# Performance work log

Measured on AMD Instinct MI355X. Metric: run time of the kernel, lower is better.

Reference implementation:

```python
import jax, jax.numpy as jnp
import numpy as np

B, CIN, H, W = 32, 128, 64, 64
OUT, KH, KW = 256, 3, 3
NSK, SDIM = 4, 128


def setup_inputs() -> dict:
    key = jax.random.key(0)
    kx, kw_, kb, ks = jax.random.split(key, 4)
    x = jax.random.normal(kx, (B, CIN, H, W), dtype=jnp.float32)
    kval = float(np.sqrt(1.0 / (CIN * KH * KW)))  # groups=1
    weight = jax.random.uniform(kw_, (OUT, CIN, KH, KW), jnp.float32, -kval, kval)
    bias_tensor = jax.random.uniform(kb, (OUT,), jnp.float32, -kval, kval)
    # Rademacher / sketch_dim, shape (n, s, O) == torch's type1_signed_matrices
    signed = (2.0 * jax.random.bernoulli(ks, 0.5, (NSK, SDIM, OUT)).astype(jnp.float32) - 1.0) / SDIM
    # prod = einsum('ijkl,mi->mjkl') per sketch -> (n, s, Cin, kh, kw)
    prod = jnp.einsum('oikl,nso->nsikl', weight, signed)
    # .permute(2,3,1,0).flatten(0,2): (s,Cin,kh,kw) -> (kh,kw,Cin,s) -> (kh*kw*Cin, s)
    type1_sketches = prod.transpose(0, 3, 4, 2, 1).reshape(NSK, KH * KW * CIN, SDIM)
    return {
        "x": x,
        "type1_sketches": type1_sketches,
        "type1_signed_matrices": signed,
        "bias_tensor": bias_tensor,
    }


def reference(x, type1_sketches, type1_signed_matrices, bias_tensor):
    b, _, h1, w1 = x.shape
    h2 = h1 - KH + 1
    w2 = w1 - KW + 1
    # torch unfold: (B, Cin*KH*KW, E), features ordered channel-major (C, kh, kw)
    patches = jax.lax.conv_general_dilated_patches(
        x, filter_shape=(KH, KW), window_strides=(1, 1), padding='VALID'
    )  # (B, Cin*KH*KW, H2, W2)
    patches = patches.reshape(b, CIN * KH * KW, h2 * w2)  # (B, F, E)
    # 'bnfe,nfs->bnse' with the n-expansion folded away
    y = jnp.einsum('bfe,nfs->bnse', patches, type1_sketches)
    z = jnp.einsum('bnse,nso->bnoe', y, type1_signed_matrices)
    z = z.reshape(b, NSK, OUT, h2, w2)
    out = jnp.mean(z, axis=1) + bias_tensor[None, :, None, None]
    return out
```

## Files before the change

kernel.cpp:

```cpp
#include <hip/hip_runtime.h>
#include <hip/hip_bf16.h>
#include <stdint.h>


#define BATCH 32
#define CIN   128
#define HH    64
#define WW    64
#define OUTC  256
#define H2    62
#define W2    62
#define A_TILE 16384
#define WS_A_BYTES (36 * A_TILE)
#define BROWB 16384

typedef __bf16 bf16x8 __attribute__((ext_vector_type(8)));
typedef float  f32x4  __attribute__((ext_vector_type(4)));

typedef unsigned int u32_as1 __attribute__((address_space(1)));
typedef unsigned int u32_as3 __attribute__((address_space(3)));

__device__ __forceinline__ void async_copy16(const void* g, void* l) {
  __builtin_amdgcn_global_load_lds((const u32_as1*)g, (u32_as3*)l, 16, 0, 0);
}

#define FPB 4
__global__ __launch_bounds__(256) void weff_kernel(
    const float* __restrict__ sketches,
    const float* __restrict__ sgn,
    char* __restrict__ wsA)
{
  __shared__ alignas(16) float sk[512 * FPB];
  const int f0 = blockIdx.x * FPB;
  const int t  = threadIdx.x;

  for (int k = 0; k < (512 * FPB) / 256; ++k) {
    int idx = t + k * 256;
    int fi  = idx >> 9;
    int ns  = idx & 511;
    int n   = ns >> 7;
    int s   = ns & 127;
    sk[ns * FPB + fi] = sketches[(n * 1152 + f0 + fi) * 128 + s];
  }
  __syncthreads();

  const int o = t;
  float acc0 = 0.f, acc1 = 0.f, acc2 = 0.f, acc3 = 0.f;
#pragma unroll 8
  for (int ns = 0; ns < 512; ++ns) {
    float sg = sgn[ns * 256 + o];
    f32x4 skv = *(const f32x4*)(&sk[ns * FPB]);
    acc0 += sg * skv[0];
    acc1 += sg * skv[1];
    acc2 += sg * skv[2];
    acc3 += sg * skv[3];
  }

  float accs[FPB] = {acc0, acc1, acc2, acc3};
#pragma unroll
  for (int fi = 0; fi < FPB; ++fi) {
    int f    = f0 + fi;
    int c    = f / 9;
    int khkw = f - c * 9;
    int st   = khkw * 4 + (c >> 5);
    int kk   = c & 31;
    uint32_t byteoff = (uint32_t)st * A_TILE + (uint32_t)o * 64
                     + (((uint32_t)kk * 2u) ^ (uint32_t)((o & 3) << 4)
                                            ^ (uint32_t)((o & 4) << 2));
    *(__hip_bfloat16*)(wsA + byteoff) = __float2bfloat16(accs[fi] * 0.25f);
  }
}

__global__ __launch_bounds__(512, 2) void conv_kernel(
    const float* __restrict__ x,
    const char*  __restrict__ wA,
    const float* __restrict__ bias,
    float* __restrict__ out)
{
  __shared__ alignas(16) char lds[3 * A_TILE + 6 * BROWB];
  char* ldsA = lds;
  char* ldsB = lds + 3 * A_TILE;

  const int bid = blockIdx.x;
  const int swz = (bid & 7) * 64 + (bid >> 3);
  const int b   = swz >> 4;
  const int ig  = swz & 15;
  const int i0  = ig * 4;

  const int t    = threadIdx.x;
  const int lane = t & 63;
  const int w    = t >> 6;
  const int wo   = w >> 2;
  const int we   = w & 3;

#define STAGE_A(ST, BUF) do {                                              \
    const char* asrc_ = wA + (size_t)(ST) * A_TILE + w * 2048 + lane * 16; \
    char* adst_ = ldsA + (BUF) * A_TILE + w * 2048;                        \
    async_copy16(asrc_,         adst_);                                    \
    async_copy16(asrc_ + 1024,  adst_ + 1024);                             \
  } while (0)

  STAGE_A(0, 0);
  STAGE_A(1, 1);

  {
    const int j  = t & 63;
    const int cq = t >> 6;
    const uint32_t swb = (uint32_t)((j & 7) << 4);
#pragma unroll
    for (int r = 0; r < 6; ++r) {
      int xrow = i0 + r; if (xrow > 63) xrow = 63;
      const float* xr = x + (((size_t)(b * CIN + cq * 16)) * HH + xrow) * WW + j;
      char* lrow = ldsB + r * BROWB + j * 256;
#pragma unroll
      for (int g = 0; g < 2; ++g) {
        bf16x8 pk;
#pragma unroll
        for (int cc = 0; cc < 8; ++cc)
          pk[cc] = (__bf16)xr[(size_t)(g * 8 + cc) * (HH * WW)];
        uint32_t c0b = (uint32_t)(cq * 32 + g * 16);
        *(bf16x8*)(lrow + (c0b ^ swb)) = pk;
      }
    }
  }

  f32x4 acc[8][4];
  const f32x4 zf = {0.f, 0.f, 0.f, 0.f};
#pragma unroll
  for (int mi = 0; mi < 8; ++mi)
#pragma unroll
    for (int ni = 0; ni < 4; ++ni)
      acc[mi][ni] = zf;

  const int ln15  = lane & 15;
  const int khi16 = (lane >> 4) << 4;
  const char* pA = ldsA + (wo * 128 + ln15) * 64
                 + (((uint32_t)khi16) ^ ((uint32_t)((ln15 & 3) << 4))
                                      ^ ((uint32_t)((ln15 & 4) << 2)));

#define MKB(COL, PAR) (ldsB + we * BROWB + (COL) * 256                     \
    + (((uint32_t)khi16) ^ ((uint32_t)(((COL) & 3) << 4)))                 \
    + (uint32_t)((((PAR) ^ (((COL) >> 2) & 1)) & 1) * 64))
  const char* pB0E = MKB(ln15 + 0, 0); const char* pB0O = MKB(ln15 + 0, 1);
  const char* pB1E = MKB(ln15 + 1, 0); const char* pB1O = MKB(ln15 + 1, 1);
  const char* pB2E = MKB(ln15 + 2, 0); const char* pB2O = MKB(ln15 + 2, 1);
  const int c30 = (48 + ln15 + 0 > 63) ? 63 : 48 + ln15 + 0;
  const int c31 = (48 + ln15 + 1 > 63) ? 63 : 48 + ln15 + 1;
  const int c32 = (48 + ln15 + 2 > 63) ? 63 : 48 + ln15 + 2;
  const char* pC0E = MKB(c30, 0); const char* pC0O = MKB(c30, 1);
  const char* pC1E = MKB(c31, 0); const char* pC1O = MKB(c31, 1);
  const char* pC2E = MKB(c32, 0); const char* pC2O = MKB(c32, 1);
#undef MKB

  asm volatile("s_waitcnt lgkmcnt(0)" ::: "memory");

#define MFMA_ __builtin_amdgcn_mfma_f32_16x16x32_bf16
#define WVM2 asm volatile("s_waitcnt vmcnt(2)" ::: "memory")
#define WVM0 asm volatile("s_waitcnt vmcnt(0)" ::: "memory")

#define STEP(ST, KH, KW, CSH, PAR, BUF, TGT, WVM) do {                     \
    WVM;                                                                   \
    __builtin_amdgcn_s_barrier();                                          \
    if ((ST) < 34) STAGE_A((ST) + 2, TGT);                                 \
    const int bimm_ = (KH) * BROWB + (CSH) * 128;                          \
    const int aimm_ = (BUF) * A_TILE;                                      \
    bf16x8 b0_ = *(const bf16x8*)(pB##KW##PAR + bimm_);                    \
    bf16x8 b1_ = *(const bf16x8*)(pB##KW##PAR + bimm_ + 4096);             \
    bf16x8 b2_ = *(const bf16x8*)(pB##KW##PAR + bimm_ + 8192);             \
    bf16x8 b3_ = *(const bf16x8*)(pC##KW##PAR + bimm_);                    \
    bf16x8 a0_ = *(const bf16x8*)(pA + aimm_);                             \
    bf16x8 a1_ = *(const bf16x8*)(pA + aimm_ + 1024);                      \
    bf16x8 a2_ = *(const bf16x8*)(pA + aimm_ + 2048);                      \
    bf16x8 a3_ = *(const bf16x8*)(pA + aimm_ + 3072);                      \
    bf16x8 a4_ = *(const bf16x8*)(pA + aimm_ + 4096);                      \
    bf16x8 a5_ = *(const bf16x8*)(pA + aimm_ + 5120);                      \
    bf16x8 a6_ = *(const bf16x8*)(pA + aimm_ + 6144);                      \
    bf16x8 a7_ = *(const bf16x8*)(pA + aimm_ + 7168);                      \
    __builtin_amdgcn_s_setprio(1);                                         \
    acc[0][0] = MFMA_(a0_, b0_, acc[0][0], 0, 0, 0);                       \
    acc[0][1] = MFMA_(a0_, b1_, acc[0][1], 0, 0, 0);                       \
    acc[0][2] = MFMA_(a0_, b2_, acc[0][2], 0, 0, 0);                       \
    acc[0][3] = MFMA_(a0_, b3_, acc[0][3], 0, 0, 0);                       \
    acc[1][0] = MFMA_(a1_, b0_, acc[1][0], 0, 0, 0);                       \
    acc[1][1] = MFMA_(a1_, b1_, acc[1][1], 0, 0, 0);                       \
    acc[1][2] = MFMA_(a1_, b2_, acc[1][2], 0, 0, 0);                       \
    acc[1][3] = MFMA_(a1_, b3_, acc[1][3], 0, 0, 0);                       \
    acc[2][0] = MFMA_(a2_, b0_, acc[2][0], 0, 0, 0);                       \
    acc[2][1] = MFMA_(a2_, b1_, acc[2][1], 0, 0, 0);                       \
    acc[2][2] = MFMA_(a2_, b2_, acc[2][2], 0, 0, 0);                       \
    acc[2][3] = MFMA_(a2_, b3_, acc[2][3], 0, 0, 0);                       \
    acc[3][0] = MFMA_(a3_, b0_, acc[3][0], 0, 0, 0);                       \
    acc[3][1] = MFMA_(a3_, b1_, acc[3][1], 0, 0, 0);                       \
    acc[3][2] = MFMA_(a3_, b2_, acc[3][2], 0, 0, 0);                       \
    acc[3][3] = MFMA_(a3_, b3_, acc[3][3], 0, 0, 0);                       \
    acc[4][0] = MFMA_(a4_, b0_, acc[4][0], 0, 0, 0);                       \
    acc[4][1] = MFMA_(a4_, b1_, acc[4][1], 0, 0, 0);                       \
    acc[4][2] = MFMA_(a4_, b2_, acc[4][2], 0, 0, 0);                       \
    acc[4][3] = MFMA_(a4_, b3_, acc[4][3], 0, 0, 0);                       \
    acc[5][0] = MFMA_(a5_, b0_, acc[5][0], 0, 0, 0);                       \
    acc[5][1] = MFMA_(a5_, b1_, acc[5][1], 0, 0, 0);                       \
    acc[5][2] = MFMA_(a5_, b2_, acc[5][2], 0, 0, 0);                       \
    acc[5][3] = MFMA_(a5_, b3_, acc[5][3], 0, 0, 0);                       \
    acc[6][0] = MFMA_(a6_, b0_, acc[6][0], 0, 0, 0);                       \
    acc[6][1] = MFMA_(a6_, b1_, acc[6][1], 0, 0, 0);                       \
    acc[6][2] = MFMA_(a6_, b2_, acc[6][2], 0, 0, 0);                       \
    acc[6][3] = MFMA_(a6_, b3_, acc[6][3], 0, 0, 0);                       \
    acc[7][0] = MFMA_(a7_, b0_, acc[7][0], 0, 0, 0);                       \
    acc[7][1] = MFMA_(a7_, b1_, acc[7][1], 0, 0, 0);                       \
    acc[7][2] = MFMA_(a7_, b2_, acc[7][2], 0, 0, 0);                       \
    acc[7][3] = MFMA_(a7_, b3_, acc[7][3], 0, 0, 0);                       \
    __builtin_amdgcn_s_setprio(0);                                         \
  } while (0)

  STEP(0,  0,0, 0,E, 0, 2, WVM2);  STEP(1,  0,0, 0,O, 1, 0, WVM2);
  STEP(2,  0,0, 1,E, 2, 1, WVM2);  STEP(3,  0,0, 1,O, 0, 2, WVM2);
  STEP(4,  0,1, 0,E, 1, 0, WVM2);  STEP(5,  0,1, 0,O, 2, 1, WVM2);
  STEP(6,  0,1, 1,E, 0, 2, WVM2);  STEP(7,  0,1, 1,O, 1, 0, WVM2);
  STEP(8,  0,2, 0,E, 2, 1, WVM2);  STEP(9,  0,2, 0,O, 0, 2, WVM2);
  STEP(10, 0,2, 1,E, 1, 0, WVM2);  STEP(11, 0,2, 1,O, 2, 1, WVM2);
  STEP(12, 1,0, 0,E, 0, 2, WVM2);  STEP(13, 1,0, 0,O, 1, 0, WVM2);
  STEP(14, 1,0, 1,E, 2, 1, WVM2);  STEP(15, 1,0, 1,O, 0, 2, WVM2);
  STEP(16, 1,1, 0,E, 1, 0, WVM2);  STEP(17, 1,1, 0,O, 2, 1, WVM2);
  STEP(18, 1,1, 1,E, 0, 2, WVM2);  STEP(19, 1,1, 1,O, 1, 0, WVM2);
  STEP(20, 1,2, 0,E, 2, 1, WVM2);  STEP(21, 1,2, 0,O, 0, 2, WVM2);
  STEP(22, 1,2, 1,E, 1, 0, WVM2);  STEP(23, 1,2, 1,O, 2, 1, WVM2);
  STEP(24, 2,0, 0,E, 0, 2, WVM2);  STEP(25, 2,0, 0,O, 1, 0, WVM2);
  STEP(26, 2,0, 1,E, 2, 1, WVM2);  STEP(27, 2,0, 1,O, 0, 2, WVM2);
  STEP(28, 2,1, 0,E, 1, 0, WVM2);  STEP(29, 2,1, 0,O, 2, 1, WVM2);
  STEP(30, 2,1, 1,E, 0, 2, WVM2);  STEP(31, 2,1, 1,O, 1, 0, WVM2);
  STEP(32, 2,2, 0,E, 2, 1, WVM2);  STEP(33, 2,2, 0,O, 0, 2, WVM2);
  STEP(34, 2,2, 1,E, 1, 0, WVM2);  STEP(35, 2,2, 1,O, 2, 1, WVM0);

#undef STEP
#undef WVM0
#undef WVM2
#undef MFMA_
#undef STAGE_A

  const int jn   = ln15;
  const int g4   = lane >> 4;
  const int irow = i0 + we;
  if (irow < H2) {
#pragma unroll
    for (int mi = 0; mi < 8; ++mi) {
#pragma unroll
      for (int ni = 0; ni < 4; ++ni) {
        const int jj = (ni << 4) + jn;
        if (jj < W2) {
#pragma unroll
          for (int rr = 0; rr < 4; ++rr) {
            const int o = (wo << 7) + (mi << 4) + (g4 << 2) + rr;
            out[(((size_t)b * OUTC + o) * H2 + irow) * W2 + jj] =
                acc[mi][ni][rr] + bias[o];
          }
        }
      }
    }
  }
}

extern "C" void kernel_launch(void* const* d_in, const int* in_sizes, int n_in,
                              void* d_out, int out_size, void* d_ws, size_t ws_size,
                              hipStream_t stream) {
  const float* x        = (const float*)d_in[0];
  const float* sketches = (const float*)d_in[1];
  const float* sgn      = (const float*)d_in[2];
  const float* bias     = (const float*)d_in[3];
  float* out            = (float*)d_out;
  char* wsA             = (char*)d_ws;

  if (ws_size < (size_t)WS_A_BYTES) return;

  weff_kernel<<<1152 / FPB, 256, 0, stream>>>(sketches, sgn, wsA);
  conv_kernel<<<BATCH * 16, 512, 0, stream>>>(x, wsA, bias, out);
}
```

Baseline: 110.0 us.

## Deepen A staging to four LDS buffers and software-pipeline fragment loads

The weight tile staging grows from triple to quadruple buffering, so global-to-LDS copies are issued three stages ahead. LDS fragment reads for the next step now go into a second register set while the current step's MFMAs run, which hides LDS latency behind matrix work. The weight-tile layout is changed to a direct per-lane contiguous layout without the XOR swizzle, which simplifies addressing. The cost is more LDS per block, which may limit two blocks per CU, and double the fragment registers, which raises register pressure under the 512x2 launch bounds.

```diff
diff --git a/kernel.cpp b/kernel.cpp
--- a/kernel.cpp
+++ b/kernel.cpp
@@ -59,14 +59,14 @@
   float accs[FPB] = {acc0, acc1, acc2, acc3};
 #pragma unroll
   for (int fi = 0; fi < FPB; ++fi) {
-    int f    = f0 + fi;
-    int c    = f / 9;
-    int khkw = f - c * 9;
-    int st   = khkw * 4 + (c >> 5);
-    int kk   = c & 31;
-    uint32_t byteoff = (uint32_t)st * A_TILE + (uint32_t)o * 64
-                     + (((uint32_t)kk * 2u) ^ (uint32_t)((o & 3) << 4)
-                                            ^ (uint32_t)((o & 4) << 2));
+    int f   = f0 + fi;
+    int c   = f / 9;
+    int tap = f - c * 9;
+    int st  = tap * 4 + (c >> 5);
+    int kk  = c & 31;
+    uint32_t byteoff = (uint32_t)st * A_TILE + (uint32_t)(o >> 4) * 1024
+                     + (uint32_t)(((kk >> 3) * 16 + (o & 15)) * 16)
+                     + (uint32_t)((kk & 7) * 2);
     *(__hip_bfloat16*)(wsA + byteoff) = __float2bfloat16(accs[fi] * 0.25f);
   }
 }
@@ -77,9 +77,9 @@
     const float* __restrict__ bias,
     float* __restrict__ out)
 {
-  __shared__ alignas(16) char lds[3 * A_TILE + 6 * BROWB];
+  __shared__ alignas(16) char lds[4 * A_TILE + 6 * BROWB];
   char* ldsA = lds;
-  char* ldsB = lds + 3 * A_TILE;
+  char* ldsB = lds + 4 * A_TILE;
 
   const int bid = blockIdx.x;
   const int swz = (bid & 7) * 64 + (bid >> 3);
@@ -102,6 +102,7 @@
 
   STAGE_A(0, 0);
   STAGE_A(1, 1);
+  STAGE_A(2, 2);
 
   {
     const int j  = t & 63;
@@ -134,9 +135,7 @@
 
   const int ln15  = lane & 15;
   const int khi16 = (lane >> 4) << 4;
-  const char* pA = ldsA + (wo * 128 + ln15) * 64
-                 + (((uint32_t)khi16) ^ ((uint32_t)((ln15 & 3) << 4))
-                                      ^ ((uint32_t)((ln15 & 4) << 2)));
+  const char* pA = ldsA + wo * 8192 + lane * 16;
 
 #define MKB(COL, PAR) (ldsB + we * BROWB + (COL) * 256                     \
     + (((uint32_t)khi16) ^ ((uint32_t)(((COL) & 3) << 4)))                 \
@@ -152,89 +151,123 @@
   const char* pC2E = MKB(c32, 0); const char* pC2O = MKB(c32, 1);
 #undef MKB
 
-  asm volatile("s_waitcnt lgkmcnt(0)" ::: "memory");
+  bf16x8 A00, A01, A02, A03, A04, A05, A06, A07, B00, B01, B02, B03;
+  bf16x8 A10, A11, A12, A13, A14, A15, A16, A17, B10, B11, B12, B13;
+
+#define PRE(P, BUF, KH, KW, PAR, CSH) do {                                 \
+    const int ab_ = (BUF) * A_TILE;                                        \
+    A##P##0 = *(const bf16x8*)(pA + ab_);                                  \
+    A##P##1 = *(const bf16x8*)(pA + ab_ + 1024);                           \
+    A##P##2 = *(const bf16x8*)(pA + ab_ + 2048);                           \
+    A##P##3 = *(const bf16x8*)(pA + ab_ + 3072);                           \
+    A##P##4 = *(const bf16x8*)(pA + ab_ + 4096);                           \
+    A##P##5 = *(const bf16x8*)(pA + ab_ + 5120);                           \
+    A##P##6 = *(const bf16x8*)(pA + ab_ + 6144);                           \
+    A##P##7 = *(const bf16x8*)(pA + ab_ + 7168);                           \
+    const int bi_ = (KH) * BROWB + (CSH) * 128;                            \
+    B##P##0 = *(const bf16x8*)(pB##KW##PAR + bi_);                         \
+    B##P##1 = *(const bf16x8*)(pB##KW##PAR + bi_ + 4096);                  \
+    B##P##2 = *(const bf16x8*)(pB##KW##PAR + bi_ + 8192);                  \
+    B##P##3 = *(const bf16x8*)(pC##KW##PAR + bi_);                         \
+  } while (0)
 
 #define MFMA_ __builtin_amdgcn_mfma_f32_16x16x32_bf16
+#define MM(P) do {                                                         \
+    __builtin_amdgcn_s_setprio(1);                                         \
+    acc[0][0] = MFMA_(A##P##0, B##P##0, acc[0][0], 0, 0, 0);               \
+    acc[0][1] = MFMA_(A##P##0, B##P##1, acc[0][1], 0, 0, 0);               \
+    acc[0][2] = MFMA_(A##P##0, B##P##2, acc[0][2], 0, 0, 0);               \
+    acc[0][3] = MFMA_(A##P##0, B##P##3, acc[0][3], 0, 0, 0);               \
+    acc[1][0] = MFMA_(A##P##1, B##P##0, acc[1][0], 0, 0, 0);               \
+    acc[1][1] = MFMA_(A##P##1, B##P##1, acc[1][1], 0, 0, 0);               \
+    acc[1][2] = MFMA_(A##P##1, B##P##2, acc[1][2], 0, 0, 0);               \
+    acc[1][3] = MFMA_(A##P##1, B##P##3, acc[1][3], 0, 0, 0);               \
+    acc[2][0] = MFMA_(A##P##2, B##P##0, acc[2][0], 0, 0, 0);               \
+    acc[2][1] = MFMA_(A##P##2, B##P##1, acc[2][1], 0, 0, 0);               \
+    acc[2][2] = MFMA_(A##P##2, B##P##2, acc[2][2], 0, 0, 0);               \
+    acc[2][3] = MFMA_(A##P##2, B##P##3, acc[2][3], 0, 0, 0);               \
+    acc[3][0] = MFMA_(A##P##3, B##P##0, acc[3][0], 0, 0, 0);               \
+    acc[3][1] = MFMA_(A##P##3, B##P##1, acc[3][1], 0, 0, 0);               \
+    acc[3][2] = MFMA_(A##P##3, B##P##2, acc[3][2], 0, 0, 0);               \
+    acc[3][3] = MFMA_(A##P##3, B##P##3, acc[3][3], 0, 0, 0);               \
+    acc[4][0] = MFMA_(A##P##4, B##P##0, acc[4][0], 0, 0, 0);               \
+    acc[4][1] = MFMA_(A##P##4, B##P##1, acc[4][1], 0, 0, 0);               \
+    acc[4][2] = MFMA_(A##P##4, B##P##2, acc[4][2], 0, 0, 0);               \
+    acc[4][3] = MFMA_(A##P##4, B##P##3, acc[4][3], 0, 0, 0);               \
+    acc[5][0] = MFMA_(A##P##5, B##P##0, acc[5][0], 0, 0, 0);               \
+    acc[5][1] = MFMA_(A##P##5, B##P##1, acc[5][1], 0, 0, 0);               \
+    acc[5][2] = MFMA_(A##P##5, B##P##2, acc[5][2], 0, 0, 0);               \
+    acc[5][3] = MFMA_(A##P##5, B##P##3, acc[5][3], 0, 0, 0);               \
+    acc[6][0] = MFMA_(A##P##6, B##P##0, acc[6][0], 0, 0, 0);               \
+    acc[6][1] = MFMA_(A##P##6, B##P##1, acc[6][1], 0, 0, 0);               \
+    acc[6][2] = MFMA_(A##P##6, B##P##2, acc[6][2], 0, 0, 0);               \
+    acc[6][3] = MFMA_(A##P##6, B##P##3, acc[6][3], 0, 0, 0);               \
+    acc[7][0] = MFMA_(A##P##7, B##P##0, acc[7][0], 0, 0, 0);               \
+    acc[7][1] = MFMA_(A##P##7, B##P##1, acc[7][1], 0, 0, 0);               \
+    acc[7][2] = MFMA_(A##P##7, B##P##2, acc[7][2], 0, 0, 0);               \
+    acc[7][3] = MFMA_(A##P##7, B##P##3, acc[7][3], 0, 0, 0);               \
+    __builtin_amdgcn_s_setprio(0);                                         \
+  } while (0)
+
 #define WVM2 asm volatile("s_waitcnt vmcnt(2)" ::: "memory")
 #define WVM0 asm volatile("s_waitcnt vmcnt(0)" ::: "memory")
 
-#define STEP(ST, KH, KW, CSH, PAR, BUF, TGT, WVM) do {                     \
+  asm volatile("s_waitcnt vmcnt(4) lgkmcnt(0)" ::: "memory");
+  __builtin_amdgcn_s_barrier();
+
+  PRE(0, 0, 0, 0, E, 0);
+
+#define STEP(ST, CUR, NXT, KH, KW, PAR, CSH, WVM) do {                     \
     WVM;                                                                   \
     __builtin_amdgcn_s_barrier();                                          \
-    if ((ST) < 34) STAGE_A((ST) + 2, TGT);                                 \
-    const int bimm_ = (KH) * BROWB + (CSH) * 128;                          \
-    const int aimm_ = (BUF) * A_TILE;                                      \
-    bf16x8 b0_ = *(const bf16x8*)(pB##KW##PAR + bimm_);                    \
-    bf16x8 b1_ = *(const bf16x8*)(pB##KW##PAR + bimm_ + 4096);             \
-    bf16x8 b2_ = *(const bf16x8*)(pB##KW##PAR + bimm_ + 8192);             \
-    bf16x8 b3_ = *(const bf16x8*)(pC##KW##PAR + bimm_);                    \
-    bf16x8 a0_ = *(const bf16x8*)(pA + aimm_);                             \
-    bf16x8 a1_ = *(const bf16x8*)(pA + aimm_ + 1024);                      \
-    bf16x8 a2_ = *(const bf16x8*)(pA + aimm_ + 2048);                      \
-    bf16x8 a3_ = *(const bf16x8*)(pA + aimm_ + 3072);                      \
-    bf16x8 a4_ = *(const bf16x8*)(pA + aimm_ + 4096);                      \
-    bf16x8 a5_ = *(const bf16x8*)(pA + aimm_ + 5120);                      \
-    bf16x8 a6_ = *(const bf16x8*)(pA + aimm_ + 6144);                      \
-    bf16x8 a7_ = *(const bf16x8*)(pA + aimm_ + 7168);                      \
-    __builtin_amdgcn_s_setprio(1);                                         \
-    acc[0][0] = MFMA_(a0_, b0_, acc[0][0], 0, 0, 0);                       \
-    acc[0][1] = MFMA_(a0_, b1_, acc[0][1], 0, 0, 0);                       \
-    acc[0][2] = MFMA_(a0_, b2_, acc[0][2], 0, 0, 0);                       \
-    acc[0][3] = MFMA_(a0_, b3_, acc[0][3], 0, 0, 0);                       \
-    acc[1][0] = MFMA_(a1_, b0_, acc[1][0], 0, 0, 0);                       \
-    acc[1][1] = MFMA_(a1_, b1_, acc[1][1], 0, 0, 0);                       \
-    acc[1][2] = MFMA_(a1_, b2_, acc[1][2], 0, 0, 0);                       \
-    acc[1][3] = MFMA_(a1_, b3_, acc[1][3], 0, 0, 0);                       \
-    acc[2][0] = MFMA_(a2_, b0_, acc[2][0], 0, 0, 0);                       \
-    acc[2][1] = MFMA_(a2_, b1_, acc[2][1], 0, 0, 0);                       \
-    acc[2][2] = MFMA_(a2_, b2_, acc[2][2], 0, 0, 0);                       \
-    acc[2][3] = MFMA_(a2_, b3_, acc[2][3], 0, 0, 0);                       \
-    acc[3][0] = MFMA_(a3_, b0_, acc[3][0], 0, 0, 0);                       \
-    acc[3][1] = MFMA_(a3_, b1_, acc[3][1], 0, 0, 0);                       \
-    acc[3][2] = MFMA_(a3_, b2_, acc[3][2], 0, 0, 0);                       \
-    acc[3][3] = MFMA_(a3_, b3_, acc[3][3], 0, 0, 0);                       \
-    acc[4][0] = MFMA_(a4_, b0_, acc[4][0], 0, 0, 0);                       \
-    acc[4][1] = MFMA_(a4_, b1_, acc[4][1], 0, 0, 0);                       \
-    acc[4][2] = MFMA_(a4_, b2_, acc[4][2], 0, 0, 0);                       \
-    acc[4][3] = MFMA_(a4_, b3_, acc[4][3], 0, 0, 0);                       \
-    acc[5][0] = MFMA_(a5_, b0_, acc[5][0], 0, 0, 0);                       \
-    acc[5][1] = MFMA_(a5_, b1_, acc[5][1], 0, 0, 0);                       \
-    acc[5][2] = MFMA_(a5_, b2_, acc[5][2], 0, 0, 0);                       \
-    acc[5][3] = MFMA_(a5_, b3_, acc[5][3], 0, 0, 0);                       \
-    acc[6][0] = MFMA_(a6_, b0_, acc[6][0], 0, 0, 0);                       \
-    acc[6][1] = MFMA_(a6_, b1_, acc[6][1], 0, 0, 0);                       \
-    acc[6][2] = MFMA_(a6_, b2_, acc[6][2], 0, 0, 0);                       \
-    acc[6][3] = MFMA_(a6_, b3_, acc[6][3], 0, 0, 0);                       \
-    acc[7][0] = MFMA_(a7_, b0_, acc[7][0], 0, 0, 0);                       \
-    acc[7][1] = MFMA_(a7_, b1_, acc[7][1], 0, 0, 0);                       \
-    acc[7][2] = MFMA_(a7_, b2_, acc[7][2], 0, 0, 0);                       \
-    acc[7][3] = MFMA_(a7_, b3_, acc[7][3], 0, 0, 0);                       \
-    __builtin_amdgcn_s_setprio(0);                                         \
+    if ((ST) + 3 <= 35) STAGE_A((ST) + 3, ((ST) + 3) & 3);                 \
+    if ((ST) < 35) PRE(NXT, ((ST) + 1) & 3, KH, KW, PAR, CSH);             \
+    MM(CUR);                                                               \
   } while (0)
 
-  STEP(0,  0,0, 0,E, 0, 2, WVM2);  STEP(1,  0,0, 0,O, 1, 0, WVM2);
-  STEP(2,  0,0, 1,E, 2, 1, WVM2);  STEP(3,  0,0, 1,O, 0, 2, WVM2);
-  STEP(4,  0,1, 0,E, 1, 0, WVM2);  STEP(5,  0,1, 0,O, 2, 1, WVM2);
-  STEP(6,  0,1, 1,E, 0, 2, WVM2);  STEP(7,  0,1, 1,O, 1, 0, WVM2);
-  STEP(8,  0,2, 0,E, 2, 1, WVM2);  STEP(9,  0,2, 0,O, 0, 2, WVM2);
-  STEP(10, 0,2, 1,E, 1, 0, WVM2);  STEP(11, 0,2, 1,O, 2, 1, WVM2);
-  STEP(12, 1,0, 0,E, 0, 2, WVM2);  STEP(13, 1,0, 0,O, 1, 0, WVM2);
-  STEP(14, 1,0, 1,E, 2, 1, WVM2);  STEP(15, 1,0, 1,O, 0, 2, WVM2);
-  STEP(16, 1,1, 0,E, 1, 0, WVM2);  STEP(17, 1,1, 0,O, 2, 1, WVM2);
-  STEP(18, 1,1, 1,E, 0, 2, WVM2);  STEP(19, 1,1, 1,O, 1, 0, WVM2);
-  STEP(20, 1,2, 0,E, 2, 1, WVM2);  STEP(21, 1,2, 0,O, 0, 2, WVM2);
-  STEP(22, 1,2, 1,E, 1, 0, WVM2);  STEP(23, 1,2, 1,O, 2, 1, WVM2);
-  STEP(24, 2,0, 0,E, 0, 2, WVM2);  STEP(25, 2,0, 0,O, 1, 0, WVM2);
-  STEP(26, 2,0, 1,E, 2, 1, WVM2);  STEP(27, 2,0, 1,O, 0, 2, WVM2);
-  STEP(28, 2,1, 0,E, 1, 0, WVM2);  STEP(29, 2,1, 0,O, 2, 1, WVM2);
-  STEP(30, 2,1, 1,E, 0, 2, WVM2);  STEP(31, 2,1, 1,O, 1, 0, WVM2);
-  STEP(32, 2,2, 0,E, 2, 1, WVM2);  STEP(33, 2,2, 0,O, 0, 2, WVM2);
-  STEP(34, 2,2, 1,E, 1, 0, WVM2);  STEP(35, 2,2, 1,O, 2, 1, WVM0);
+  STEP(0,  0, 1,  0, 0, O, 0, WVM2);
+  STEP(1,  1, 0,  0, 0, E, 1, WVM2);
+  STEP(2,  0, 1,  0, 0, O, 1, WVM2);
+  STEP(3,  1, 0,  0, 1, E, 0, WVM2);
+  STEP(4,  0, 1,  0, 1, O, 0, WVM2);
+  STEP(5,  1, 0,  0, 1, E, 1, WVM2);
+  STEP(6,  0, 1,  0, 1, O, 1, WVM2);
+  STEP(7,  1, 0,  0, 2, E, 0, WVM2);
+  STEP(8,  0, 1,  0, 2, O, 0, WVM2);
+  STEP(9,  1, 0,  0, 2, E, 1, WVM2);
+  STEP(10, 0, 1,  0, 2, O, 1, WVM2);
+  STEP(11, 1, 0,  1, 0, E, 0, WVM2);
+  STEP(12, 0, 1,  1, 0, O, 0, WVM2);
+  STEP(13, 1, 0,  1, 0, E, 1, WVM2);
+  STEP(14, 0, 1,  1, 0, O, 1, WVM2);
+  STEP(15, 1, 0,  1, 1, E, 0, WVM2);
+  STEP(16, 0, 1,  1, 1, O, 0, WVM2);
+  STEP(17, 1, 0,  1, 1, E, 1, WVM2);
+  STEP(18, 0, 1,  1, 1, O, 1, WVM2);
+  STEP(19, 1, 0,  1, 2, E, 0, WVM2);
+  STEP(20, 0, 1,  1, 2, O, 0, WVM2);
+  STEP(21, 1, 0,  1, 2, E, 1, WVM2);
+  STEP(22, 0, 1,  1, 2, O, 1, WVM2);
+  STEP(23, 1, 0,  2, 0, E, 0, WVM2);
+  STEP(24, 0, 1,  2, 0, O, 0, WVM2);
+  STEP(25, 1, 0,  2, 0, E, 1, WVM2);
+  STEP(26, 0, 1,  2, 0, O, 1, WVM2);
+  STEP(27, 1, 0,  2, 1, E, 0, WVM2);
+  STEP(28, 0, 1,  2, 1, O, 0, WVM2);
+  STEP(29, 1, 0,  2, 1, E, 1, WVM2);
+  STEP(30, 0, 1,  2, 1, O, 1, WVM2);
+  STEP(31, 1, 0,  2, 2, E, 0, WVM2);
+  STEP(32, 0, 1,  2, 2, O, 0, WVM2);
+  STEP(33, 1, 0,  2, 2, E, 1, WVM2);
+  STEP(34, 0, 1,  2, 2, O, 1, WVM0);
+  MM(1);
 
 #undef STEP
 #undef WVM0
 #undef WVM2
+#undef MM
 #undef MFMA_
+#undef PRE
 #undef STAGE_A
 
   const int jn   = ln15;
```

Result: faster. 105.0 us (-4.5%).
